# Performance work log

Measured on AMD Instinct MI355X. Metric: run time of the kernel, lower is better.

The kernel has to match this reference:

```python
import jax, jax.numpy as jnp
import numpy as np

IN_FEATURES = 512
OUT_FEATURES = 100000
BATCH = 1024
MARGIN = 0.5
SCALE = 20.0


def setup_inputs() -> dict:
    key = jax.random.key(0)
    k1, k2, k3 = jax.random.split(key, 3)
    features = jax.random.normal(k1, (BATCH, IN_FEATURES), dtype=jnp.float32)
    targets = jax.random.randint(k2, (BATCH,), 0, OUT_FEATURES, dtype=jnp.int64)
    # xavier_normal_ for [out, in]: std = sqrt(2/(fan_in+fan_out))
    std = float(np.sqrt(2.0 / (IN_FEATURES + OUT_FEATURES)))
    weights = jax.random.normal(k3, (OUT_FEATURES, IN_FEATURES), dtype=jnp.float32) * std
    return {"features": features, "targets": targets, "weights": weights}


def _l2_normalize(x, axis=-1, eps=1e-12):
    # Matches torch F.normalize(p=2): x / max(||x||, eps)
    norm = jnp.linalg.norm(x, axis=axis, keepdims=True)
    return x / jnp.maximum(norm, eps)


def reference(features, targets, weights):
    f = _l2_normalize(features, axis=1)            # [B, D]
    w = _l2_normalize(weights, axis=1)             # [C, D]
    cos_theta = jnp.einsum('bd,cd->bc', f, w)      # [B, C]
    cos_theta = jnp.clip(cos_theta, -1.0, 1.0)
    arc_cos = jnp.arccos(cos_theta)
    # add margin only at target class (scatter-style, no dense one_hot matmul)
    rows = jnp.arange(arc_cos.shape[0])
    arc_cos = arc_cos.at[rows, targets].add(MARGIN)
    logits = jnp.cos(arc_cos) * SCALE
    return logits
```

## Files before the change

### kernel.cpp

```cpp
#include <hip/hip_runtime.h>
#include <cstdint>
#include <cstddef>

#define IN_F   512
#define OUT_F  100000
#define BATCH_N 1024
#define BM 128
#define BN 128
#define BK 32

#define SCALE_F 20.0f
#define COS_M 0.8775825618903728f
#define SIN_M 0.4794255386042030f

typedef short s16x8 __attribute__((ext_vector_type(8)));
typedef float f32x4 __attribute__((ext_vector_type(4)));

__device__ __forceinline__ unsigned int f2bf_bits(float x) {
  union { float f; unsigned int u; } v; v.f = x;
  return (v.u + 0x7fffu + ((v.u >> 16) & 1u)) >> 16;
}

__global__ __launch_bounds__(256) void normalize_rows_bf16(
    const float* __restrict__ in, unsigned short* __restrict__ out, int rows) {
  const int gw   = (int)((blockIdx.x * 256u + threadIdx.x) >> 6);
  const int lane = threadIdx.x & 63;
  if (gw >= rows) return;
  const f32x4* rp = (const f32x4*)(in + (size_t)gw * IN_F);
  f32x4 a = __builtin_nontemporal_load(rp + lane);
  f32x4 b = __builtin_nontemporal_load(rp + lane + 64);
  float s = a.x*a.x + a.y*a.y + a.z*a.z + a.w*a.w
          + b.x*b.x + b.y*b.y + b.z*b.z + b.w*b.w;
  #pragma unroll
  for (int off = 32; off > 0; off >>= 1) s += __shfl_xor(s, off, 64);
  const float sc = 1.0f / fmaxf(sqrtf(s), 1e-12f);
  uint2 q0, q1;
  q0.x = f2bf_bits(a.x * sc) | (f2bf_bits(a.y * sc) << 16);
  q0.y = f2bf_bits(a.z * sc) | (f2bf_bits(a.w * sc) << 16);
  q1.x = f2bf_bits(b.x * sc) | (f2bf_bits(b.y * sc) << 16);
  q1.y = f2bf_bits(b.z * sc) | (f2bf_bits(b.w * sc) << 16);
  uint2* op = (uint2*)(out + (size_t)gw * IN_F);
  op[lane]      = q0;
  op[lane + 64] = q1;
}

__global__ __launch_bounds__(256) void arcface_gemm(
    const unsigned short* __restrict__ A,
    const unsigned short* __restrict__ B,
    const int* __restrict__ targets,
    float* __restrict__ out) {
  __shared__ unsigned short As[BM * BK];
  __shared__ unsigned short Bs[BN * BK];
  __shared__ int s_tgt[BM];

  const int tid  = threadIdx.x;
  const int lane = tid & 63;
  const int wid  = tid >> 6;
  const int wm   = wid >> 1;
  const int wn   = wid & 1;

  const int L    = (int)(blockIdx.x + gridDim.x * blockIdx.y);
  const int cpx  = (int)(gridDim.x * gridDim.y) >> 3;
  const int newL = (L & 7) * cpx + (L >> 3);
  const int m0   = (newL & 7) * BM;
  const int n0   = (newL >> 3) * BN;

  if (tid < BM) s_tgt[tid] = targets[m0 + tid];

  f32x4 acc[4][4];
  const f32x4 zero = {0.f, 0.f, 0.f, 0.f};
  #pragma unroll
  for (int i = 0; i < 4; ++i)
    #pragma unroll
    for (int j = 0; j < 4; ++j) acc[i][j] = zero;

  const int lrow = lane >> 2;
  const int lcol = (lane & 3) * 8;
  const int ra0  = wid * 16;

  const int lc = lane & 15;
  const int lq = lane >> 4;
  const int kq = lq * 8;

  for (int kt = 0; kt < IN_F / BK; ++kt) {
    const int k0 = kt * BK;
    if (kt) __syncthreads();

    {
      const unsigned short* g0 = A + (size_t)(m0 + ra0 + lrow) * IN_F + k0 + lcol;
      __builtin_amdgcn_global_load_lds(
          (const __attribute__((address_space(1))) void*)g0,
          (__attribute__((address_space(3))) void*)&As[ra0 * BK], 16, 0, 0);
      const unsigned short* g1 = A + (size_t)(m0 + ra0 + 64 + lrow) * IN_F + k0 + lcol;
      __builtin_amdgcn_global_load_lds(
          (const __attribute__((address_space(1))) void*)g1,
          (__attribute__((address_space(3))) void*)&As[(ra0 + 64) * BK], 16, 0, 0);
    }
    {
      int nr0 = n0 + ra0 + lrow;       if (nr0 >= OUT_F) nr0 = OUT_F - 1;
      const unsigned short* g0 = B + (size_t)nr0 * IN_F + k0 + lcol;
      __builtin_amdgcn_global_load_lds(
          (const __attribute__((address_space(1))) void*)g0,
          (__attribute__((address_space(3))) void*)&Bs[ra0 * BK], 16, 0, 0);
      int nr1 = n0 + ra0 + 64 + lrow;  if (nr1 >= OUT_F) nr1 = OUT_F - 1;
      const unsigned short* g1 = B + (size_t)nr1 * IN_F + k0 + lcol;
      __builtin_amdgcn_global_load_lds(
          (const __attribute__((address_space(1))) void*)g1,
          (__attribute__((address_space(3))) void*)&Bs[(ra0 + 64) * BK], 16, 0, 0);
    }
    __builtin_amdgcn_s_waitcnt(0x0f70);
    __syncthreads();

    s16x8 afr[4], bfr[4];
    #pragma unroll
    for (int i = 0; i < 4; ++i)
      afr[i] = *(const s16x8*)&As[(wm * 64 + i * 16 + lc) * BK + kq];
    #pragma unroll
    for (int j = 0; j < 4; ++j)
      bfr[j] = *(const s16x8*)&Bs[(wn * 64 + j * 16 + lc) * BK + kq];
    #pragma unroll
    for (int i = 0; i < 4; ++i)
      #pragma unroll
      for (int j = 0; j < 4; ++j)
        acc[i][j] = __builtin_amdgcn_mfma_f32_16x16x32_bf16(afr[i], bfr[j], acc[i][j], 0, 0, 0);
  }

  const int cbase = n0 + wn * 64;
  #pragma unroll
  for (int i = 0; i < 4; ++i) {
    #pragma unroll
    for (int r = 0; r < 4; ++r) {
      const int lrw = wm * 64 + i * 16 + lq * 4 + r;
      const int tgt = s_tgt[lrw];
      float* orow = out + (size_t)(m0 + lrw) * OUT_F;
      #pragma unroll
      for (int j = 0; j < 4; ++j) {
        const int col = cbase + j * 16 + lc;
        if (col >= OUT_F) continue;
        float x = acc[i][j][r];
        x = fminf(1.0f, fmaxf(-1.0f, x));
        float y = (col == tgt)
                    ? (x * COS_M - sqrtf(fmaxf(1.0f - x * x, 0.0f)) * SIN_M)
                    : x;
        __builtin_nontemporal_store(SCALE_F * y, &orow[col]);
      }
    }
  }
}

extern "C" void kernel_launch(void* const* d_in, const int* in_sizes, int n_in,
                              void* d_out, int out_size, void* d_ws, size_t ws_size,
                              hipStream_t stream) {
  const float* features = (const float*)d_in[0];
  const int*   targets  = (const int*)d_in[1];
  const float* weights  = (const float*)d_in[2];
  float* out = (float*)d_out;

  unsigned short* fbf = (unsigned short*)d_ws;
  unsigned short* wbf = fbf + (size_t)BATCH_N * IN_F;

  normalize_rows_bf16<<<(BATCH_N * 64 + 255) / 256, 256, 0, stream>>>(features, fbf, BATCH_N);
  normalize_rows_bf16<<<(OUT_F * 64 + 255) / 256, 256, 0, stream>>>(weights, wbf, OUT_F);

  dim3 grid(BATCH_N / BM, (OUT_F + BN - 1) / BN);
  arcface_gemm<<<grid, 256, 0, stream>>>(fbf, wbf, targets, out);
}
```

Measured before the change: 650.0 us.

## Fuse weight normalization into GEMM by loading fp32 weights and scaling in epilogue

Removes the separate weight-normalization pass and loads fp32 weights straight in the GEMM main loop. Each tile converts them to bf16 with a hardware packed convert, stores them to LDS, and accumulates per-row squared norms. The inverse norm is applied to the accumulator in the epilogue. This avoids writing and re-reading a bf16 copy of the 100000x512 weight matrix, but each column tile now reads fp32 weights (twice the bytes) from all 8 M-blocks, and the B loads become register-staged instead of direct-to-LDS. Normalization now happens after bf16 rounding of the unnormalized weights, which slightly changes numerics.

```diff
diff --git a/kernel.cpp b/kernel.cpp
--- a/kernel.cpp
+++ b/kernel.cpp
@@ -15,10 +15,17 @@
 
 typedef short s16x8 __attribute__((ext_vector_type(8)));
 typedef float f32x4 __attribute__((ext_vector_type(4)));
+typedef unsigned int u32x4 __attribute__((ext_vector_type(4)));
 
 __device__ __forceinline__ unsigned int f2bf_bits(float x) {
   union { float f; unsigned int u; } v; v.f = x;
   return (v.u + 0x7fffu + ((v.u >> 16) & 1u)) >> 16;
+}
+
+__device__ __forceinline__ unsigned int cvt_pk_bf16(float lo, float hi) {
+  unsigned int r;
+  asm("v_cvt_pk_bf16_f32 %0, %1, %2" : "=v"(r) : "v"(lo), "v"(hi));
+  return r;
 }
 
 __global__ __launch_bounds__(256) void normalize_rows_bf16(
@@ -27,8 +34,8 @@
   const int lane = threadIdx.x & 63;
   if (gw >= rows) return;
   const f32x4* rp = (const f32x4*)(in + (size_t)gw * IN_F);
-  f32x4 a = __builtin_nontemporal_load(rp + lane);
-  f32x4 b = __builtin_nontemporal_load(rp + lane + 64);
+  f32x4 a = rp[lane];
+  f32x4 b = rp[lane + 64];
   float s = a.x*a.x + a.y*a.y + a.z*a.z + a.w*a.w
           + b.x*b.x + b.y*b.y + b.z*b.z + b.w*b.w;
   #pragma unroll
@@ -46,12 +53,13 @@
 
 __global__ __launch_bounds__(256) void arcface_gemm(
     const unsigned short* __restrict__ A,
-    const unsigned short* __restrict__ B,
+    const float* __restrict__ W,
     const int* __restrict__ targets,
     float* __restrict__ out) {
   __shared__ unsigned short As[BM * BK];
   __shared__ unsigned short Bs[BN * BK];
-  __shared__ int s_tgt[BM];
+  __shared__ int   s_tgt[BM];
+  __shared__ float s_inv[BN];
 
   const int tid  = threadIdx.x;
   const int lane = tid & 63;
@@ -82,8 +90,21 @@
   const int lq = lane >> 4;
   const int kq = lq * 8;
 
+  int nr0 = n0 + ra0 + lrow;       if (nr0 >= OUT_F) nr0 = OUT_F - 1;
+  int nr1 = n0 + ra0 + 64 + lrow;  if (nr1 >= OUT_F) nr1 = OUT_F - 1;
+  const float* wp0 = W + (size_t)nr0 * IN_F + lcol;
+  const float* wp1 = W + (size_t)nr1 * IN_F + lcol;
+
+  float ss0 = 0.0f, ss1 = 0.0f;
+
   for (int kt = 0; kt < IN_F / BK; ++kt) {
     const int k0 = kt * BK;
+
+    f32x4 u0 = *(const f32x4*)(wp0 + k0);
+    f32x4 u1 = *(const f32x4*)(wp0 + k0 + 4);
+    f32x4 v0 = *(const f32x4*)(wp1 + k0);
+    f32x4 v1 = *(const f32x4*)(wp1 + k0 + 4);
+
     if (kt) __syncthreads();
 
     {
@@ -96,19 +117,18 @@
           (const __attribute__((address_space(1))) void*)g1,
           (__attribute__((address_space(3))) void*)&As[(ra0 + 64) * BK], 16, 0, 0);
     }
-    {
-      int nr0 = n0 + ra0 + lrow;       if (nr0 >= OUT_F) nr0 = OUT_F - 1;
-      const unsigned short* g0 = B + (size_t)nr0 * IN_F + k0 + lcol;
-      __builtin_amdgcn_global_load_lds(
-          (const __attribute__((address_space(1))) void*)g0,
-          (__attribute__((address_space(3))) void*)&Bs[ra0 * BK], 16, 0, 0);
-      int nr1 = n0 + ra0 + 64 + lrow;  if (nr1 >= OUT_F) nr1 = OUT_F - 1;
-      const unsigned short* g1 = B + (size_t)nr1 * IN_F + k0 + lcol;
-      __builtin_amdgcn_global_load_lds(
-          (const __attribute__((address_space(1))) void*)g1,
-          (__attribute__((address_space(3))) void*)&Bs[(ra0 + 64) * BK], 16, 0, 0);
-    }
-    __builtin_amdgcn_s_waitcnt(0x0f70);
+
+    ss0 += u0.x*u0.x + u0.y*u0.y + u0.z*u0.z + u0.w*u0.w
+         + u1.x*u1.x + u1.y*u1.y + u1.z*u1.z + u1.w*u1.w;
+    ss1 += v0.x*v0.x + v0.y*v0.y + v0.z*v0.z + v0.w*v0.w
+         + v1.x*v1.x + v1.y*v1.y + v1.z*v1.z + v1.w*v1.w;
+    u32x4 pb0 = { cvt_pk_bf16(u0.x, u0.y), cvt_pk_bf16(u0.z, u0.w),
+                  cvt_pk_bf16(u1.x, u1.y), cvt_pk_bf16(u1.z, u1.w) };
+    *(u32x4*)&Bs[(ra0 + lrow) * BK + lcol] = pb0;
+    u32x4 pb1 = { cvt_pk_bf16(v0.x, v0.y), cvt_pk_bf16(v0.z, v0.w),
+                  cvt_pk_bf16(v1.x, v1.y), cvt_pk_bf16(v1.z, v1.w) };
+    *(u32x4*)&Bs[(ra0 + 64 + lrow) * BK + lcol] = pb1;
+
     __syncthreads();
 
     s16x8 afr[4], bfr[4];
@@ -125,7 +145,18 @@
         acc[i][j] = __builtin_amdgcn_mfma_f32_16x16x32_bf16(afr[i], bfr[j], acc[i][j], 0, 0, 0);
   }
 
+  ss0 += __shfl_xor(ss0, 1, 64);  ss0 += __shfl_xor(ss0, 2, 64);
+  ss1 += __shfl_xor(ss1, 1, 64);  ss1 += __shfl_xor(ss1, 2, 64);
+  if ((lane & 3) == 0) {
+    s_inv[ra0 + lrow]      = 1.0f / fmaxf(sqrtf(ss0), 1e-12f);
+    s_inv[ra0 + 64 + lrow] = 1.0f / fmaxf(sqrtf(ss1), 1e-12f);
+  }
+  __syncthreads();
+
   const int cbase = n0 + wn * 64;
+  float winv[4];
+  #pragma unroll
+  for (int j = 0; j < 4; ++j) winv[j] = s_inv[wn * 64 + j * 16 + lc];
   #pragma unroll
   for (int i = 0; i < 4; ++i) {
     #pragma unroll
@@ -137,7 +168,7 @@
       for (int j = 0; j < 4; ++j) {
         const int col = cbase + j * 16 + lc;
         if (col >= OUT_F) continue;
-        float x = acc[i][j][r];
+        float x = acc[i][j][r] * winv[j];
         x = fminf(1.0f, fmaxf(-1.0f, x));
         float y = (col == tgt)
                     ? (x * COS_M - sqrtf(fmaxf(1.0f - x * x, 0.0f)) * SIN_M)
@@ -157,11 +188,9 @@
   float* out = (float*)d_out;
 
   unsigned short* fbf = (unsigned short*)d_ws;
-  unsigned short* wbf = fbf + (size_t)BATCH_N * IN_F;
 
   normalize_rows_bf16<<<(BATCH_N * 64 + 255) / 256, 256, 0, stream>>>(features, fbf, BATCH_N);
-  normalize_rows_bf16<<<(OUT_F * 64 + 255) / 256, 256, 0, stream>>>(weights, wbf, OUT_F);
 
   dim3 grid(BATCH_N / BM, (OUT_F + BN - 1) / BN);
-  arcface_gemm<<<grid, 256, 0, stream>>>(fbf, wbf, targets, out);
+  arcface_gemm<<<grid, 256, 0, stream>>>(fbf, weights, targets, out);
 }
```

New measurement: 773.4 us. 1.19x slower.
